# Kernel optimization log

Measured on AMD Instinct MI355X. Metric: run time of the kernel, lower is better.

The kernel has to match this reference:

```python
import jax, jax.numpy as jnp
import numpy as np

B, S, HID = 2, 2048, 2048
NH, NG = 32, 8
HD = HID // NH  # 64
KV = HD * NG    # 512


def setup_inputs() -> dict:
    key = jax.random.key(0)
    ks = jax.random.split(key, 9)
    w = lambda k, shp: jax.random.normal(k, shp, dtype=jnp.float32) * 0.02
    return {
        "hidden_state": jax.random.normal(ks[0], (B, S, HID), dtype=jnp.float32),
        "Wq": w(ks[1], (HID, HID)), "bq": jnp.zeros((HID,), jnp.float32),
        "Wk": w(ks[2], (HID, KV)),  "bk": jnp.zeros((KV,), jnp.float32),
        "Wv": w(ks[3], (HID, KV)),  "bv": jnp.zeros((KV,), jnp.float32),
        "Wo": w(ks[4], (HID, HID)), "bo": jnp.zeros((HID,), jnp.float32),
    }


def reference(hidden_state, Wq, bq, Wk, bk, Wv, bv, Wo, bo):
    bs, seq, _ = hidden_state.shape
    rep = NH // NG  # heads per KV group

    q = hidden_state @ Wq + bq                      # [B,S,HID]
    k = hidden_state @ Wk + bk                      # [B,S,KV]
    v = hidden_state @ Wv + bv

    q = q.reshape(bs, seq, NH, HD).transpose(0, 2, 1, 3)   # [B,NH,S,D]
    k = k.reshape(bs, seq, NG, HD).transpose(0, 2, 1, 3)   # [B,NG,S,D]
    v = v.reshape(bs, seq, NG, HD).transpose(0, 2, 1, 3)
    # grouped-KV expansion: each group repeated consecutively rep times
    k = jnp.repeat(k, rep, axis=1)                          # [B,NH,S,D]
    v = jnp.repeat(v, rep, axis=1)

    scores = jnp.einsum("bhqd,bhkd->bhqk", q, k) / jnp.sqrt(jnp.float32(HD))
    probs = jax.nn.softmax(scores, axis=-1)
    out = jnp.einsum("bhqk,bhkd->bhqd", probs, v)           # [B,NH,S,D]
    out = out.transpose(0, 2, 1, 3).reshape(bs, seq, HID)
    return out @ Wo + bo
```

## Files before the change

kernel.cpp:

```cpp
#include <hip/hip_runtime.h>
#include <hip/hip_bf16.h>
#include <math.h>

typedef __bf16 bf16x8 __attribute__((ext_vector_type(8)));
typedef float f32x4 __attribute__((ext_vector_type(4)));
typedef __hip_bfloat16 bf16_t;

#define MFMA_BF16(a, b, c) __builtin_amdgcn_mfma_f32_16x16x32_bf16((a), (b), (c), 0, 0, 0)

__device__ __forceinline__ void async_copy16(const bf16_t* g, bf16_t* lds_base) {
  __builtin_amdgcn_global_load_lds(
      (const __attribute__((address_space(1))) unsigned int*)g,
      (__attribute__((address_space(3))) unsigned int*)lds_base,
      16, 0, 0);
}

__device__ __forceinline__ unsigned fbits(float x) { return __builtin_bit_cast(unsigned, x); }

__global__ __launch_bounds__(256) void prep(
    const float* __restrict__ hidden, const float* __restrict__ Wq, const float* __restrict__ Wk,
    const float* __restrict__ Wv, const float* __restrict__ Wo,
    const float* __restrict__ bq, const float* __restrict__ bk, const float* __restrict__ bv,
    bf16_t* __restrict__ hiddenB, bf16_t* __restrict__ WqkvT, bf16_t* __restrict__ WoT,
    float* __restrict__ bqkv, float c1) {
  __shared__ float tile[64][65];
  int bid = blockIdx.x;
  const int t = threadIdx.x;
  if (bid < 8192) {
    const int i = bid * 256 + t;
    float4 v = ((const float4*)hidden)[i];
    union { bf16_t h[4]; ushort4 u; } cv;
    cv.h[0] = __float2bfloat16(v.x);
    cv.h[1] = __float2bfloat16(v.y);
    cv.h[2] = __float2bfloat16(v.z);
    cv.h[3] = __float2bfloat16(v.w);
    ((ushort4*)hiddenB)[i] = cv.u;
    return;
  }
  bid -= 8192;
  if (bid >= 2560) {
    const int i = (bid - 2560) * 256 + t;
    float v;
    if (i < 2048) v = bq[i] * c1;
    else if (i < 2560) v = bk[i - 2048];
    else v = bv[i - 2560];
    bqkv[i] = v;
    return;
  }
  const float* src;
  bf16_t* dst;
  int Cc, bx, by;
  float scale = 1.0f;
  if (bid < 1024) { src = Wq; dst = WqkvT; Cc = 2048; bx = bid & 31; by = bid >> 5; scale = c1; }
  else if (bid < 1280) { bid -= 1024; src = Wk; dst = WqkvT + (size_t)2048 * 2048; Cc = 512; bx = bid & 7; by = bid >> 3; }
  else if (bid < 1536) { bid -= 1280; src = Wv; dst = WqkvT + (size_t)2560 * 2048; Cc = 512; bx = bid & 7; by = bid >> 3; }
  else { bid -= 1536; src = Wo; dst = WoT; Cc = 2048; bx = bid & 31; by = bid >> 5; }
  const int tx = t & 63, ty = t >> 6;
  const int c0 = bx * 64, r0 = by * 64;
#pragma unroll
  for (int i = ty; i < 64; i += 4)
    tile[i][tx] = src[(size_t)(r0 + i) * Cc + c0 + tx];
  __syncthreads();
#pragma unroll
  for (int i = ty; i < 64; i += 4)
    dst[(size_t)(c0 + i) * 2048 + r0 + tx] = __float2bfloat16(tile[tx][i] * scale);
}

template <typename TOUT>
__global__ __launch_bounds__(256, 3) void gemm_bt(
    const bf16_t* __restrict__ A, const bf16_t* __restrict__ Bt,
    const float* __restrict__ bias, TOUT* __restrict__ C, bf16_t* __restrict__ vTp,
    int M, int N, int K) {
  __shared__ alignas(16) bf16_t As[128 * 64];
  __shared__ alignas(16) bf16_t Bs[128 * 64];

  const int tid = threadIdx.x;
  const int w = tid >> 6, lane = tid & 63;
  const int quad = lane >> 4, l16 = lane & 15;
  const int wm = w >> 1, wn = w & 1;
  const int m0 = blockIdx.y * 128, n0 = blockIdx.x * 128;

  f32x4 acc[4][4] = {};

  const int rr = lane >> 3;
  const int scol = ((lane & 7) ^ rr) * 8;
  const int sx = l16 & 7;

  for (int k0 = 0; k0 < K; k0 += 64) {
    __syncthreads();
#pragma unroll
    for (int c = 0; c < 4; ++c) {
      const int r = w * 32 + c * 8 + rr;
      async_copy16(A + (size_t)(m0 + r) * K + k0 + scol, &As[(w * 32 + c * 8) * 64]);
      async_copy16(Bt + (size_t)(n0 + r) * K + k0 + scol, &Bs[(w * 32 + c * 8) * 64]);
    }
    __syncthreads();

#pragma unroll
    for (int kh = 0; kh < 2; ++kh) {
      bf16x8 af[4], bf[4];
#pragma unroll
      for (int i = 0; i < 4; ++i) {
        af[i] = *(const bf16x8*)&As[(wm * 64 + i * 16 + l16) * 64 + (((kh * 4 + quad) ^ sx) * 8)];
        bf[i] = *(const bf16x8*)&Bs[(wn * 64 + i * 16 + l16) * 64 + (((kh * 4 + quad) ^ sx) * 8)];
      }
#pragma unroll
      for (int i = 0; i < 4; ++i)
#pragma unroll
        for (int j = 0; j < 4; ++j)
          acc[i][j] = MFMA_BF16(af[i], bf[j], acc[i][j]);
    }
  }

  if (vTp != nullptr && n0 >= 2560) {
#pragma unroll
    for (int i = 0; i < 4; ++i) {
      const int row = m0 + wm * 64 + i * 16 + quad * 4;
      const int bb = row >> 11, s = row & 2047;
#pragma unroll
      for (int j = 0; j < 4; ++j) {
        const int col = n0 + wn * 64 + j * 16 + l16;
        const float bv = bias[col];
        union { bf16_t h[4]; ushort4 u; } cv;
#pragma unroll
        for (int r = 0; r < 4; ++r) cv.h[r] = __float2bfloat16(acc[i][j][r] + bv);
        *(ushort4*)&vTp[((size_t)bb * 512 + (col - 2560)) * 2048 + s] = cv.u;
      }
    }
    return;
  }

#pragma unroll
  for (int i = 0; i < 4; ++i) {
    const int row = m0 + wm * 64 + i * 16 + quad * 4;
#pragma unroll
    for (int j = 0; j < 4; ++j) {
      const int col = n0 + wn * 64 + j * 16 + l16;
      const float bv = bias[col];
#pragma unroll
      for (int r = 0; r < 4; ++r) {
        const float val = acc[i][j][r] + bv;
        if constexpr (__is_same(TOUT, float)) {
          C[(size_t)(row + r) * N + col] = val;
        } else {
          C[(size_t)(row + r) * N + col] = __float2bfloat16(val);
        }
      }
    }
  }
}

__global__ __launch_bounds__(256, 4) void gqa_attn(
    const bf16_t* __restrict__ QKV, const bf16_t* __restrict__ VT, bf16_t* __restrict__ O) {
  constexpr int S = 2048, HID = 2048, QKVS = 3072, HD = 64;
  const int tid = threadIdx.x;
  const int w = tid >> 6, lane = tid & 63;
  const int quad = lane >> 4, l16 = lane & 15;
  const int hp = blockIdx.y, b = blockIdx.z;
  const int h = hp * 2 + (w & 1);
  const int g = hp >> 1;
  const int q0 = blockIdx.x * 64 + (w >> 1) * 32;

  __shared__ alignas(16) bf16_t Ks[64 * 64];
  __shared__ alignas(16) bf16_t VTs[64 * 64];
  __shared__ alignas(16) bf16_t Ps[128 * 64];

  bf16x8 qf[2][2];
#pragma unroll
  for (int mt = 0; mt < 2; ++mt)
#pragma unroll
    for (int ks = 0; ks < 2; ++ks)
      qf[mt][ks] = *(const bf16x8*)&QKV[(size_t)(b * S + q0 + mt * 16 + l16) * QKVS +
                                        h * HD + ks * 32 + quad * 8];

  const int rr = lane >> 3, c7 = lane & 7;
  const int scol = (c7 ^ rr) * 8;
  const int sx = l16 & 7;

  const bf16_t* Kbase = QKV + (size_t)b * S * QKVS + 2048 + g * HD;
  const bf16_t* Vbase = VT + (size_t)(b * 512 + g * HD) * S;

  f32x4 oacc[2][4] = {};
  f32x4 lacc[2] = {};
  bf16x8 ones;
#pragma unroll
  for (int j = 0; j < 8; ++j) ones[j] = (__bf16)1.0f;

  for (int s0 = 0; s0 < S; s0 += 64) {
    __syncthreads();
#pragma unroll
    for (int cg = 0; cg < 2; ++cg) {
      const int r = w * 16 + cg * 8 + rr;
      async_copy16(Kbase + (size_t)(s0 + r) * QKVS + scol, &Ks[(w * 16 + cg * 8) * 64]);
      async_copy16(Vbase + (size_t)r * S + s0 + scol, &VTs[(w * 16 + cg * 8) * 64]);
    }
    __syncthreads();

#pragma unroll
    for (int nt = 0; nt < 4; ++nt) {
      bf16x8 kf0 = *(const bf16x8*)&Ks[(nt * 16 + l16) * 64 + ((quad ^ sx) * 8)];
      bf16x8 kf1 = *(const bf16x8*)&Ks[(nt * 16 + l16) * 64 + (((4 + quad) ^ sx) * 8)];
#pragma unroll
      for (int mt = 0; mt < 2; ++mt) {
        f32x4 s = {};
        s = MFMA_BF16(kf0, qf[mt][0], s);
        s = MFMA_BF16(kf1, qf[mt][1], s);
        const float p0 = __builtin_amdgcn_exp2f(s[0]);
        const float p1 = __builtin_amdgcn_exp2f(s[1]);
        const float p2 = __builtin_amdgcn_exp2f(s[2]);
        const float p3 = __builtin_amdgcn_exp2f(s[3]);
        uint2 pk;
        pk.x = __builtin_amdgcn_perm(fbits(p1), fbits(p0), 0x07060302);
        pk.y = __builtin_amdgcn_perm(fbits(p3), fbits(p2), 0x07060302);
        *(uint2*)&Ps[(w * 32 + mt * 16 + l16) * 64 +
                     (((nt * 2 + (quad >> 1)) ^ sx) * 8) + (quad & 1) * 4] = pk;
      }
    }

#pragma unroll
    for (int kc = 0; kc < 2; ++kc) {
      bf16x8 pf[2];
#pragma unroll
      for (int mt = 0; mt < 2; ++mt) {
        pf[mt] = *(const bf16x8*)&Ps[(w * 32 + mt * 16 + l16) * 64 + (((kc * 4 + quad) ^ sx) * 8)];
        lacc[mt] = MFMA_BF16(pf[mt], ones, lacc[mt]);
      }
#pragma unroll
      for (int dt = 0; dt < 4; ++dt) {
        bf16x8 vf = *(const bf16x8*)&VTs[(dt * 16 + l16) * 64 + (((kc * 4 + quad) ^ sx) * 8)];
#pragma unroll
        for (int mt = 0; mt < 2; ++mt)
          oacc[mt][dt] = MFMA_BF16(pf[mt], vf, oacc[mt][dt]);
      }
    }
  }

#pragma unroll
  for (int mt = 0; mt < 2; ++mt) {
    float linv[4];
#pragma unroll
    for (int r = 0; r < 4; ++r) linv[r] = 1.0f / lacc[mt][r];
#pragma unroll
    for (int dt = 0; dt < 4; ++dt)
#pragma unroll
      for (int r = 0; r < 4; ++r)
        O[(size_t)(b * S + q0 + mt * 16 + quad * 4 + r) * HID + h * HD + dt * 16 + l16] =
            __float2bfloat16(oacc[mt][dt][r] * linv[r]);
  }
}

extern "C" void kernel_launch(void* const* d_in, const int* in_sizes, int n_in,
                              void* d_out, int out_size, void* d_ws, size_t ws_size,
                              hipStream_t stream) {
  const float* hidden = (const float*)d_in[0];
  const float* Wq = (const float*)d_in[1];
  const float* bq = (const float*)d_in[2];
  const float* Wk = (const float*)d_in[3];
  const float* bk = (const float*)d_in[4];
  const float* Wv = (const float*)d_in[5];
  const float* bv = (const float*)d_in[6];
  const float* Wo = (const float*)d_in[7];
  const float* bo = (const float*)d_in[8];
  float* out = (float*)d_out;

  constexpr int B = 2, S = 2048, HID = 2048, KV = 512, QKVN = 3072;
  constexpr int M = B * S;
  const float c1 = 0.125f * 1.44269504089f;

  char* ws = (char*)d_ws;
  bf16_t* hiddenB = (bf16_t*)ws; ws += (size_t)M * HID * 2;
  bf16_t* WqkvT = (bf16_t*)ws;   ws += (size_t)QKVN * HID * 2;
  bf16_t* WoT = (bf16_t*)ws;     ws += (size_t)HID * HID * 2;
  bf16_t* qkv = (bf16_t*)ws;     ws += (size_t)M * QKVN * 2;
  bf16_t* vT = (bf16_t*)ws;      ws += (size_t)M * KV * 2;
  bf16_t* attn = (bf16_t*)ws;    ws += (size_t)M * HID * 2;
  float* bqkv = (float*)ws;      ws += QKVN * 4;

  prep<<<8192 + 2560 + 12, 256, 0, stream>>>(hidden, Wq, Wk, Wv, Wo, bq, bk, bv,
                                             hiddenB, WqkvT, WoT, bqkv, c1);

  gemm_bt<bf16_t><<<dim3(QKVN / 128, M / 128), 256, 0, stream>>>(
      hiddenB, WqkvT, bqkv, qkv, vT, M, QKVN, HID);

  gqa_attn<<<dim3(S / 64, 16, B), 256, 0, stream>>>(qkv, vT, attn);

  gemm_bt<float><<<dim3(HID / 128, M / 128), 256, 0, stream>>>(
      attn, WoT, bo, out, (bf16_t*)nullptr, M, HID, HID);
}
```

Baseline: 290.7 us.

## Register-prefetch next K/V tile instead of synchronous global-to-LDS copies

Replaces the direct global_load_lds async copies of each K/V tile, which were waited on immediately, with a register-staged software pipeline. Each iteration writes the previously loaded registers into swizzled LDS, then issues global loads for the next tile so their latency overlaps the MFMA compute. The compute section is also raised to higher wave priority with s_setprio. The cost is extra VGPRs for the staged tile, and the final iteration issues a wasted wrap-around load of tile zero.

Result: slower. 302.5 us (+4.1%).

```diff
diff --git a/kernel.cpp b/kernel.cpp
--- a/kernel.cpp
+++ b/kernel.cpp
@@ -174,11 +174,20 @@
                                         h * HD + ks * 32 + quad * 8];
 
   const int rr = lane >> 3, c7 = lane & 7;
-  const int scol = (c7 ^ rr) * 8;
   const int sx = l16 & 7;
 
   const bf16_t* Kbase = QKV + (size_t)b * S * QKVS + 2048 + g * HD;
   const bf16_t* Vbase = VT + (size_t)(b * 512 + g * HD) * S;
+
+  const int srow = w * 16 + rr;
+  const bf16_t* kp0 = Kbase + (size_t)srow * QKVS + c7 * 8;
+  const bf16_t* kp1 = kp0 + (size_t)8 * QKVS;
+  const bf16_t* vp0 = Vbase + (size_t)srow * S + c7 * 8;
+  const bf16_t* vp1 = vp0 + (size_t)8 * S;
+  bf16_t* KsW0 = &Ks[(srow)*64 + (c7 ^ rr) * 8];
+  bf16_t* KsW1 = KsW0 + 8 * 64;
+  bf16_t* VsW0 = &VTs[(srow)*64 + (c7 ^ rr) * 8];
+  bf16_t* VsW1 = VsW0 + 8 * 64;
 
   f32x4 oacc[2][4] = {};
   f32x4 lacc[2] = {};
@@ -186,16 +195,25 @@
 #pragma unroll
   for (int j = 0; j < 8; ++j) ones[j] = (__bf16)1.0f;
 
+  uint4 kr0 = *(const uint4*)kp0;
+  uint4 kr1 = *(const uint4*)kp1;
+  uint4 vr0 = *(const uint4*)vp0;
+  uint4 vr1 = *(const uint4*)vp1;
+
   for (int s0 = 0; s0 < S; s0 += 64) {
     __syncthreads();
-#pragma unroll
-    for (int cg = 0; cg < 2; ++cg) {
-      const int r = w * 16 + cg * 8 + rr;
-      async_copy16(Kbase + (size_t)(s0 + r) * QKVS + scol, &Ks[(w * 16 + cg * 8) * 64]);
-      async_copy16(Vbase + (size_t)r * S + s0 + scol, &VTs[(w * 16 + cg * 8) * 64]);
-    }
+    *(uint4*)KsW0 = kr0;
+    *(uint4*)KsW1 = kr1;
+    *(uint4*)VsW0 = vr0;
+    *(uint4*)VsW1 = vr1;
+    const int sn = (s0 + 64) & (S - 1);
+    kr0 = *(const uint4*)(kp0 + (size_t)sn * QKVS);
+    kr1 = *(const uint4*)(kp1 + (size_t)sn * QKVS);
+    vr0 = *(const uint4*)(vp0 + sn);
+    vr1 = *(const uint4*)(vp1 + sn);
     __syncthreads();
 
+    __builtin_amdgcn_s_setprio(1);
 #pragma unroll
     for (int nt = 0; nt < 4; ++nt) {
       bf16x8 kf0 = *(const bf16x8*)&Ks[(nt * 16 + l16) * 64 + ((quad ^ sx) * 8)];
@@ -233,6 +251,7 @@
           oacc[mt][dt] = MFMA_BF16(pf[mt], vf, oacc[mt][dt]);
       }
     }
+    __builtin_amdgcn_s_setprio(0);
   }
 
 #pragma unroll
```

## Double-buffer attention KV tiles, share across all group heads, swizzle GEMM blocks

Applied to the files above, without the earlier changes.

The attention kernel now runs 512-thread blocks that cover all four heads of a KV group, so each K/V tile is loaded once per group instead of once per head pair. It replaces async global-to-LDS copies with register prefetch into double-buffered LDS, which leaves one barrier per iteration and raises wave priority during the MFMA section. The GEMM remaps block indices with an XCD-style swizzle to improve cache locality. These changes use more LDS and registers per block, which may lower occupancy.

Result: slower. 300.0 us (+3.2%).

```diff
diff --git a/kernel.cpp b/kernel.cpp
--- a/kernel.cpp
+++ b/kernel.cpp
@@ -78,7 +78,11 @@
   const int w = tid >> 6, lane = tid & 63;
   const int quad = lane >> 4, l16 = lane & 15;
   const int wm = w >> 1, wn = w & 1;
-  const int m0 = blockIdx.y * 128, n0 = blockIdx.x * 128;
+
+  const int nwg = gridDim.x * gridDim.y;
+  const int flat = blockIdx.y * gridDim.x + blockIdx.x;
+  const int swz = (flat & 7) * (nwg >> 3) + (flat >> 3);
+  const int m0 = (swz / gridDim.x) * 128, n0 = (swz % gridDim.x) * 128;
 
   f32x4 acc[4][4] = {};
 
@@ -150,20 +154,19 @@
   }
 }
 
-__global__ __launch_bounds__(256, 4) void gqa_attn(
+__global__ __launch_bounds__(512, 2) void gqa_attn(
     const bf16_t* __restrict__ QKV, const bf16_t* __restrict__ VT, bf16_t* __restrict__ O) {
   constexpr int S = 2048, HID = 2048, QKVS = 3072, HD = 64;
   const int tid = threadIdx.x;
   const int w = tid >> 6, lane = tid & 63;
   const int quad = lane >> 4, l16 = lane & 15;
-  const int hp = blockIdx.y, b = blockIdx.z;
-  const int h = hp * 2 + (w & 1);
-  const int g = hp >> 1;
-  const int q0 = blockIdx.x * 64 + (w >> 1) * 32;
-
-  __shared__ alignas(16) bf16_t Ks[64 * 64];
-  __shared__ alignas(16) bf16_t VTs[64 * 64];
-  __shared__ alignas(16) bf16_t Ps[128 * 64];
+  const int g = blockIdx.y, b = blockIdx.z;
+  const int h = g * 4 + (w & 3);
+  const int q0 = blockIdx.x * 64 + (w >> 2) * 32;
+
+  __shared__ alignas(16) bf16_t Ks[2 * 64 * 64];
+  __shared__ alignas(16) bf16_t VTs[2 * 64 * 64];
+  __shared__ alignas(16) bf16_t Ps[256 * 64];
 
   bf16x8 qf[2][2];
 #pragma unroll
@@ -174,11 +177,15 @@
                                         h * HD + ks * 32 + quad * 8];
 
   const int rr = lane >> 3, c7 = lane & 7;
-  const int scol = (c7 ^ rr) * 8;
   const int sx = l16 & 7;
 
   const bf16_t* Kbase = QKV + (size_t)b * S * QKVS + 2048 + g * HD;
   const bf16_t* Vbase = VT + (size_t)(b * 512 + g * HD) * S;
+
+  const int srow = w * 8 + rr;
+  const bf16_t* kp = Kbase + (size_t)srow * QKVS + c7 * 8;
+  const bf16_t* vp = Vbase + (size_t)srow * S + c7 * 8;
+  const int woff = srow * 64 + (c7 ^ rr) * 8;
 
   f32x4 oacc[2][4] = {};
   f32x4 lacc[2] = {};
@@ -186,20 +193,23 @@
 #pragma unroll
   for (int j = 0; j < 8; ++j) ones[j] = (__bf16)1.0f;
 
-  for (int s0 = 0; s0 < S; s0 += 64) {
+  uint4 kr = *(const uint4*)kp;
+  uint4 vr = *(const uint4*)vp;
+
+  for (int it = 0; it < 32; ++it) {
+    const int cur = (it & 1) * (64 * 64);
+    *(uint4*)&Ks[cur + woff] = kr;
+    *(uint4*)&VTs[cur + woff] = vr;
+    const int sn = ((it + 1) & 31) * 64;
+    kr = *(const uint4*)(kp + (size_t)sn * QKVS);
+    vr = *(const uint4*)(vp + sn);
     __syncthreads();
-#pragma unroll
-    for (int cg = 0; cg < 2; ++cg) {
-      const int r = w * 16 + cg * 8 + rr;
-      async_copy16(Kbase + (size_t)(s0 + r) * QKVS + scol, &Ks[(w * 16 + cg * 8) * 64]);
-      async_copy16(Vbase + (size_t)r * S + s0 + scol, &VTs[(w * 16 + cg * 8) * 64]);
-    }
-    __syncthreads();
-
+
+    __builtin_amdgcn_s_setprio(1);
 #pragma unroll
     for (int nt = 0; nt < 4; ++nt) {
-      bf16x8 kf0 = *(const bf16x8*)&Ks[(nt * 16 + l16) * 64 + ((quad ^ sx) * 8)];
-      bf16x8 kf1 = *(const bf16x8*)&Ks[(nt * 16 + l16) * 64 + (((4 + quad) ^ sx) * 8)];
+      bf16x8 kf0 = *(const bf16x8*)&Ks[cur + (nt * 16 + l16) * 64 + ((quad ^ sx) * 8)];
+      bf16x8 kf1 = *(const bf16x8*)&Ks[cur + (nt * 16 + l16) * 64 + (((4 + quad) ^ sx) * 8)];
 #pragma unroll
       for (int mt = 0; mt < 2; ++mt) {
         f32x4 s = {};
@@ -227,12 +237,13 @@
       }
 #pragma unroll
       for (int dt = 0; dt < 4; ++dt) {
-        bf16x8 vf = *(const bf16x8*)&VTs[(dt * 16 + l16) * 64 + (((kc * 4 + quad) ^ sx) * 8)];
+        bf16x8 vf = *(const bf16x8*)&VTs[cur + (dt * 16 + l16) * 64 + (((kc * 4 + quad) ^ sx) * 8)];
 #pragma unroll
         for (int mt = 0; mt < 2; ++mt)
           oacc[mt][dt] = MFMA_BF16(pf[mt], vf, oacc[mt][dt]);
       }
     }
+    __builtin_amdgcn_s_setprio(0);
   }
 
 #pragma unroll
@@ -282,7 +293,7 @@
   gemm_bt<bf16_t><<<dim3(QKVN / 128, M / 128), 256, 0, stream>>>(
       hiddenB, WqkvT, bqkv, qkv, vT, M, QKVN, HID);
 
-  gqa_attn<<<dim3(S / 64, 16, B), 256, 0, stream>>>(qkv, vT, attn);
+  gqa_attn<<<dim3(S / 64, 8, B), 512, 0, stream>>>(qkv, vT, attn);
 
   gemm_bt<float><<<dim3(HID / 128, M / 128), 256, 0, stream>>>(
       attn, WoT, bo, out, (bf16_t*)nullptr, M, HID, HID);
```
